# Performance work log

Measured on AMD Instinct MI355X. Metric: run time of the kernel, lower is better.

## Reference

```python
import jax, jax.numpy as jnp
import numpy as np

B, T, L, D = 4, 32, 64, 768
NHEAD, DFF, NLAYERS, NSPK = 12, 2048, 2, 4
DH = D // NHEAD


def setup_inputs() -> dict:
    key = jax.random.key(0)
    ks = jax.random.split(key, 12)
    s = 0.02
    return {
        "token_embeddings": jax.random.normal(ks[0], (B, T, L, D), jnp.float32) * s,
        "speaker_ids": jax.random.randint(ks[1], (B, T), 0, NSPK, jnp.int32),
        "Wq": jax.random.normal(ks[2], (D, D), jnp.float32) * s,
        "Wk": jax.random.normal(ks[3], (D, D), jnp.float32) * s,
        "Wv": jax.random.normal(ks[4], (D, D), jnp.float32) * s,
        "in_proj_w": jax.random.normal(ks[5], (NLAYERS, 3 * D, D), jnp.float32) * s,
        "in_proj_b": jnp.zeros((NLAYERS, 3 * D), jnp.float32),
        "out_w": jax.random.normal(ks[6], (NLAYERS, D, D), jnp.float32) * s,
        "out_b": jnp.zeros((NLAYERS, D), jnp.float32),
        "ln1_g": jnp.ones((NLAYERS, D), jnp.float32),
        "ln1_b": jnp.zeros((NLAYERS, D), jnp.float32),
        "ff1_w": jax.random.normal(ks[7], (NLAYERS, DFF, D), jnp.float32) * s,
        "ff1_b": jnp.zeros((NLAYERS, DFF), jnp.float32),
        "ff2_w": jax.random.normal(ks[8], (NLAYERS, D, DFF), jnp.float32) * s,
        "ff2_b": jnp.zeros((NLAYERS, D), jnp.float32),
        "ln2_g": jnp.ones((NLAYERS, D), jnp.float32),
        "ln2_b": jnp.zeros((NLAYERS, D), jnp.float32),
    }


def _layer_norm(x, g, b, eps=1e-5):
    mu = x.mean(-1, keepdims=True)
    var = ((x - mu) ** 2).mean(-1, keepdims=True)
    return (x - mu) * jax.lax.rsqrt(var + eps) * g + b


def _mha(x, w_in, b_in, w_out, b_out):
    # x: (N, L, D); torch nn.MultiheadAttention with in_proj/out_proj
    N, Lx, _ = x.shape
    qkv = x @ w_in.T + b_in  # (N, L, 3D)
    q, k, v = jnp.split(qkv, 3, axis=-1)
    def heads(z):
        return z.reshape(N, Lx, NHEAD, DH).transpose(0, 2, 1, 3)  # (N,H,L,dh)
    q, k, v = heads(q), heads(k), heads(v)
    scores = jnp.einsum("nhqd,nhkd->nhqk", q, k) / jnp.sqrt(jnp.float32(DH))
    attn = jax.nn.softmax(scores, axis=-1)
    out = jnp.einsum("nhqk,nhkd->nhqd", attn, v)
    out = out.transpose(0, 2, 1, 3).reshape(N, Lx, D)
    return out @ w_out.T + b_out


def reference(token_embeddings, speaker_ids, Wq, Wk, Wv, in_proj_w, in_proj_b,
              out_w, out_b, ln1_g, ln1_b, ff1_w, ff1_b, ff2_w, ff2_b, ln2_g, ln2_b):
    # edu embeddings: mean over token dim (frozen-BERT output stand-in)
    edu = token_embeddings.mean(axis=2)              # (B,T,D)
    tok = token_embeddings @ Wq.T                    # query_proj on tokens (B,T,L,D)
    k = edu @ Wk.T                                   # (B,T,D)
    v = edu @ Wv.T                                   # (B,T,D)
    # SAUTE: per-speaker causal cumulative sum of outer products k_u v_u^T
    same_spk = speaker_ids[:, :, None] == speaker_ids[:, None, :]
    causal = jnp.arange(T)[None, :, None] >= jnp.arange(T)[None, None, :]
    maskf = (same_spk & causal).astype(k.dtype)      # (B,T,T)
    M = jnp.einsum("btu,bui,buj->btij", maskf, k, v)  # (B,T,D,D) speaker state
    ctx = tok + jnp.einsum("btij,btlj->btli", M, tok)  # (B,T,L,D)
    # stacked post-norm TransformerEncoder (torch defaults: ReLU, dff=2048)
    x = ctx.reshape(B * T, L, D)
    for l in range(NLAYERS):
        a = _mha(x, in_proj_w[l], in_proj_b[l], out_w[l], out_b[l])
        x = _layer_norm(x + a, ln1_g[l], ln1_b[l])
        f = jax.nn.relu(x @ ff1_w[l].T + ff1_b[l]) @ ff2_w[l].T + ff2_b[l]
        x = _layer_norm(x + f, ln2_g[l], ln2_b[l])
    return x.reshape(B, T, L, D)
```

## Files before the change

kernel.cpp:

```cpp
#include <hip/hip_runtime.h>
#include <hip/hip_bf16.h>

#define BB 4
#define TT 32
#define LL 64
#define DD 768
#define NHEAD 12
#define DH 64
#define DFF 2048
#define NLAYERS 2
#define ROWS (BB*TT*LL)
#define BTN  (BB*TT)

typedef __attribute__((ext_vector_type(8))) short bf16x8;
typedef __attribute__((ext_vector_type(4))) float f32x4;

__device__ __forceinline__ int swz(int r, int c) {
    return r * 32 + ((c ^ ((r >> 1) & 3)) << 3);
}

__device__ __forceinline__ unsigned pack_bf16(float a, float b) {
    __hip_bfloat16 h0 = __float2bfloat16(a);
    __hip_bfloat16 h1 = __float2bfloat16(b);
    return (unsigned)*reinterpret_cast<unsigned short*>(&h0) |
           ((unsigned)*reinterpret_cast<unsigned short*>(&h1) << 16);
}

__device__ __forceinline__ short bf16s(float a) {
    __hip_bfloat16 h = __float2bfloat16(a);
    return *reinterpret_cast<short*>(&h);
}

struct CastArgs {
    const float* src[7];
    __hip_bfloat16* dst[7];
    int end[7];
};
__global__ __launch_bounds__(256) void cast_multi_kernel(CastArgs a)
{
    int q = blockIdx.x * 256 + threadIdx.x;
    if (q >= a.end[6]) return;
    int s = 0;
    while (q >= a.end[s]) ++s;
    int local = q - (s ? a.end[s - 1] : 0);
    float4 v = reinterpret_cast<const float4*>(a.src[s])[local];
    ushort4 o;
    __hip_bfloat16 h0 = __float2bfloat16(v.x);
    __hip_bfloat16 h1 = __float2bfloat16(v.y);
    __hip_bfloat16 h2 = __float2bfloat16(v.z);
    __hip_bfloat16 h3 = __float2bfloat16(v.w);
    o.x = *reinterpret_cast<unsigned short*>(&h0);
    o.y = *reinterpret_cast<unsigned short*>(&h1);
    o.z = *reinterpret_cast<unsigned short*>(&h2);
    o.w = *reinterpret_cast<unsigned short*>(&h3);
    reinterpret_cast<ushort4*>(a.dst[s])[local] = o;
}

__global__ __launch_bounds__(256) void te_prep_kernel(
    const float* __restrict__ te, __hip_bfloat16* __restrict__ teb,
    __hip_bfloat16* __restrict__ edu_b)
{
    int idx = blockIdx.x * 256 + threadIdx.x;
    int bt = idx / DD;
    int d  = idx - bt * DD;
    const float* p = te + ((size_t)bt * LL) * DD + d;
    __hip_bfloat16* q = teb + ((size_t)bt * LL) * DD + d;
    float s = 0.f;
#pragma unroll
    for (int l = 0; l < LL; ++l) {
        float v = p[(size_t)l * DD];
        s += v;
        q[(size_t)l * DD] = __float2bfloat16(v);
    }
    edu_b[idx] = __float2bfloat16(s * (1.0f / (float)LL));
}

template<int OUT_BF16, int RELU, int QKV>
__global__ __launch_bounds__(256) void gemm_bf16_kernel(
    const __hip_bfloat16* __restrict__ A,
    const __hip_bfloat16* __restrict__ B,
    const float* __restrict__ bias,
    void* __restrict__ Cout,
    __hip_bfloat16* __restrict__ Vout,
    int M, int N, int K, int ldC)
{
    __shared__ short lA[2][4096];
    __shared__ short lB[2][4096];
    const int tid  = threadIdx.x;
    const int lane = tid & 63;
    const int w    = tid >> 6;
    const int wr   = w >> 1, wc = w & 1;
    const int bm = blockIdx.y * 128;
    const int bn = blockIdx.x * 128;

    const int sr  = tid >> 2;
    const int cw  = tid & 3;
    const int sco = cw << 3;

    const int wo0 = swz(sr, cw);
    const int wo1 = swz(sr + 64, cw);
    int roA[4], roB[4];
#pragma unroll
    for (int m = 0; m < 4; ++m)
        roA[m] = swz(wr * 64 + m * 16 + (lane & 15), lane >> 4);
#pragma unroll
    for (int n = 0; n < 4; ++n)
        roB[n] = swz(wc * 64 + n * 16 + (lane & 15), lane >> 4);

    const short* Ag = reinterpret_cast<const short*>(A);
    const short* Bg = reinterpret_cast<const short*>(B);

    f32x4 acc[4][4] = {};

    bf16x8 ra0 = *reinterpret_cast<const bf16x8*>(Ag + (size_t)(bm + sr) * K + sco);
    bf16x8 ra1 = *reinterpret_cast<const bf16x8*>(Ag + (size_t)(bm + 64 + sr) * K + sco);
    bf16x8 rb0 = *reinterpret_cast<const bf16x8*>(Bg + (size_t)(bn + sr) * K + sco);
    bf16x8 rb1 = *reinterpret_cast<const bf16x8*>(Bg + (size_t)(bn + 64 + sr) * K + sco);
    *reinterpret_cast<bf16x8*>(&lA[0][wo0]) = ra0;
    *reinterpret_cast<bf16x8*>(&lA[0][wo1]) = ra1;
    *reinterpret_cast<bf16x8*>(&lB[0][wo0]) = rb0;
    *reinterpret_cast<bf16x8*>(&lB[0][wo1]) = rb1;
    __syncthreads();

    const int NT = K >> 5;
    int cur = 0;
    for (int t = 0; t < NT; ++t) {
        const bool nx = (t + 1 < NT);
        if (nx) {
            const int kn = (t + 1) << 5;
            ra0 = *reinterpret_cast<const bf16x8*>(Ag + (size_t)(bm + sr) * K + kn + sco);
            ra1 = *reinterpret_cast<const bf16x8*>(Ag + (size_t)(bm + 64 + sr) * K + kn + sco);
            rb0 = *reinterpret_cast<const bf16x8*>(Bg + (size_t)(bn + sr) * K + kn + sco);
            rb1 = *reinterpret_cast<const bf16x8*>(Bg + (size_t)(bn + 64 + sr) * K + kn + sco);
        }

        bf16x8 af[4], bfr[4];
#pragma unroll
        for (int m = 0; m < 4; ++m)
            af[m] = *reinterpret_cast<const bf16x8*>(&lA[cur][roA[m]]);
#pragma unroll
        for (int n = 0; n < 4; ++n)
            bfr[n] = *reinterpret_cast<const bf16x8*>(&lB[cur][roB[n]]);
#pragma unroll
        for (int m = 0; m < 4; ++m)
#pragma unroll
            for (int n = 0; n < 4; ++n)
                acc[m][n] = __builtin_amdgcn_mfma_f32_16x16x32_bf16(
                    af[m], bfr[n], acc[m][n], 0, 0, 0);

        if (nx) {
            *reinterpret_cast<bf16x8*>(&lA[cur ^ 1][wo0]) = ra0;
            *reinterpret_cast<bf16x8*>(&lA[cur ^ 1][wo1]) = ra1;
            *reinterpret_cast<bf16x8*>(&lB[cur ^ 1][wo0]) = rb0;
            *reinterpret_cast<bf16x8*>(&lB[cur ^ 1][wo1]) = rb1;
        }
        __syncthreads();
        cur ^= 1;
    }

    const int crow = (lane >> 4) * 4;
    const int ccol = lane & 15;
#pragma unroll
    for (int n = 0; n < 4; ++n) {
        const int col = bn + wc * 64 + n * 16 + ccol;
        const float bv = bias ? bias[col] : 0.f;
        if (QKV && col >= 1536) {
            const int hh = (col - 1536) >> 6;
            const int d  = (col - 1536) & 63;
#pragma unroll
            for (int m = 0; m < 4; ++m) {
                const int row0 = bm + wr * 64 + m * 16 + crow;
#pragma unroll
                for (int j = 0; j < 4; ++j) {
                    const int row = row0 + j;
                    const int ni = row >> 6, ll = row & 63;
                    Vout[(((size_t)ni * NHEAD + hh) << 12) + (d << 6) + ll] =
                        __float2bfloat16(acc[m][n][j] + bv);
                }
            }
        } else {
#pragma unroll
            for (int m = 0; m < 4; ++m) {
                const int row0 = bm + wr * 64 + m * 16 + crow;
#pragma unroll
                for (int j = 0; j < 4; ++j) {
                    float v = acc[m][n][j] + bv;
                    if (RELU) v = fmaxf(v, 0.f);
                    if (OUT_BF16)
                        reinterpret_cast<__hip_bfloat16*>(Cout)[(size_t)(row0 + j) * ldC + col] =
                            __float2bfloat16(v);
                    else
                        reinterpret_cast<float*>(Cout)[(size_t)(row0 + j) * ldC + col] = v;
                }
            }
        }
    }
}

__global__ __launch_bounds__(64) void attn_mfma_kernel(
    const __hip_bfloat16* __restrict__ qk,
    const __hip_bfloat16* __restrict__ vt,
    __hip_bfloat16* __restrict__ out)
{
    const int n = blockIdx.x, h = blockIdx.y;
    const int lane = threadIdx.x;
    const int lo = lane & 15, hi = lane >> 4;
    __shared__ short pl[64 * 72];

    const short* qg = reinterpret_cast<const short*>(qk) + (size_t)(n * 64) * 1536 + h * 64;

    f32x4 acc[4][4] = {};
#pragma unroll
    for (int ks = 0; ks < 2; ++ks) {
        const int kc = ks * 32 + hi * 8;
        bf16x8 af[4], bk[4];
#pragma unroll
        for (int m = 0; m < 4; ++m)
            af[m] = *reinterpret_cast<const bf16x8*>(qg + (size_t)(m * 16 + lo) * 1536 + kc);
#pragma unroll
        for (int nn = 0; nn < 4; ++nn)
            bk[nn] = *reinterpret_cast<const bf16x8*>(qg + 768 + (size_t)(nn * 16 + lo) * 1536 + kc);
#pragma unroll
        for (int m = 0; m < 4; ++m)
#pragma unroll
            for (int nn = 0; nn < 4; ++nn)
                acc[m][nn] = __builtin_amdgcn_mfma_f32_16x16x32_bf16(
                    af[m], bk[nn], acc[m][nn], 0, 0, 0);
    }

#pragma unroll
    for (int m = 0; m < 4; ++m) {
#pragma unroll
        for (int j = 0; j < 4; ++j) {
            float s0 = acc[m][0][j] * 0.125f;
            float s1 = acc[m][1][j] * 0.125f;
            float s2 = acc[m][2][j] * 0.125f;
            float s3 = acc[m][3][j] * 0.125f;
            float mx = fmaxf(fmaxf(s0, s1), fmaxf(s2, s3));
            mx = fmaxf(mx, __shfl_xor(mx, 1));
            mx = fmaxf(mx, __shfl_xor(mx, 2));
            mx = fmaxf(mx, __shfl_xor(mx, 4));
            mx = fmaxf(mx, __shfl_xor(mx, 8));
            float e0 = __expf(s0 - mx), e1 = __expf(s1 - mx);
            float e2 = __expf(s2 - mx), e3 = __expf(s3 - mx);
            float sm = e0 + e1 + e2 + e3;
            sm += __shfl_xor(sm, 1);
            sm += __shfl_xor(sm, 2);
            sm += __shfl_xor(sm, 4);
            sm += __shfl_xor(sm, 8);
            const float inv = 1.0f / sm;
            short* pr = &pl[(m * 16 + hi * 4 + j) * 72 + lo];
            pr[0]  = bf16s(e0 * inv);
            pr[16] = bf16s(e1 * inv);
            pr[32] = bf16s(e2 * inv);
            pr[48] = bf16s(e3 * inv);
        }
    }
    __syncthreads();

    const short* vg = reinterpret_cast<const short*>(vt) + ((size_t)(n * NHEAD + h) << 12);
    f32x4 o[4][4] = {};
#pragma unroll
    for (int ks = 0; ks < 2; ++ks) {
        const int kc = ks * 32 + hi * 8;
        bf16x8 pa[4], bv[4];
#pragma unroll
        for (int m = 0; m < 4; ++m)
            pa[m] = *reinterpret_cast<const bf16x8*>(&pl[(m * 16 + lo) * 72 + kc]);
#pragma unroll
        for (int nn = 0; nn < 4; ++nn)
            bv[nn] = *reinterpret_cast<const bf16x8*>(vg + (nn * 16 + lo) * 64 + kc);
#pragma unroll
        for (int m = 0; m < 4; ++m)
#pragma unroll
            for (int nn = 0; nn < 4; ++nn)
                o[m][nn] = __builtin_amdgcn_mfma_f32_16x16x32_bf16(
                    pa[m], bv[nn], o[m][nn], 0, 0, 0);
    }

#pragma unroll
    for (int m = 0; m < 4; ++m)
#pragma unroll
        for (int nn = 0; nn < 4; ++nn)
#pragma unroll
            for (int j = 0; j < 4; ++j)
                out[(size_t)(n * 64 + m * 16 + hi * 4 + j) * DD + h * 64 + nn * 16 + lo] =
                    __float2bfloat16(o[m][nn][j]);
}

__global__ __launch_bounds__(64) void saute_p_mfma_kernel(
    const __hip_bfloat16* __restrict__ Xb,
    const __hip_bfloat16* __restrict__ KV,
    const int* __restrict__ spk,
    __hip_bfloat16* __restrict__ P)
{
    const int lane = threadIdx.x;
    const int lo = lane & 15, hi = lane >> 4;
    const int row0 = blockIdx.x * 64;
    const int bt = row0 >> 6;
    const int b  = bt >> 5, t = bt & 31;

    const short* Ag = reinterpret_cast<const short*>(Xb) + (size_t)row0 * DD;
    const short* Bg = reinterpret_cast<const short*>(KV) + (size_t)(b * TT) * 1536 + 768;

    f32x4 acc[4][2] = {};
    for (int ks = 0; ks < 24; ++ks) {
        const int kc = ks * 32 + hi * 8;
        bf16x8 af[4], bv[2];
#pragma unroll
        for (int m = 0; m < 4; ++m)
            af[m] = *reinterpret_cast<const bf16x8*>(Ag + (size_t)(m * 16 + lo) * DD + kc);
#pragma unroll
        for (int nn = 0; nn < 2; ++nn)
            bv[nn] = *reinterpret_cast<const bf16x8*>(Bg + (size_t)(nn * 16 + lo) * 1536 + kc);
#pragma unroll
        for (int m = 0; m < 4; ++m)
#pragma unroll
            for (int nn = 0; nn < 2; ++nn)
                acc[m][nn] = __builtin_amdgcn_mfma_f32_16x16x32_bf16(
                    af[m], bv[nn], acc[m][nn], 0, 0, 0);
    }

    const int st = spk[bt];
#pragma unroll
    for (int nn = 0; nn < 2; ++nn) {
        const int u = nn * 16 + lo;
        const bool mk = (u <= t) && (spk[b * TT + u] == st);
#pragma unroll
        for (int m = 0; m < 4; ++m)
#pragma unroll
            for (int j = 0; j < 4; ++j) {
                const int row = row0 + m * 16 + hi * 4 + j;
                P[(size_t)row * 32 + u] =
                    mk ? __float2bfloat16(acc[m][nn][j]) : __float2bfloat16(0.f);
            }
    }
}

__global__ __launch_bounds__(256) void saute_ctx_kernel(
    __hip_bfloat16* __restrict__ Xb,
    const __hip_bfloat16* __restrict__ KV,
    const __hip_bfloat16* __restrict__ P)
{
    __shared__ unsigned kls[32 * 384];
    __shared__ float pls[8 * 32];
    const int row0 = blockIdx.x * 8;
    const int b = row0 >> 11;
    const int tid = threadIdx.x;

    const unsigned* k2 = reinterpret_cast<const unsigned*>(KV) + (size_t)(b * TT) * 768;
    for (int i = tid; i < 32 * 384; i += 256) {
        int u = i / 384, j = i - u * 384;
        kls[i] = k2[u * 768 + j];
    }
    pls[tid] = __bfloat162float(P[(size_t)row0 * 32 + tid]);
    __syncthreads();

    const int r = tid >> 5;
    const int l32 = tid & 31;
    unsigned* xrow = reinterpret_cast<unsigned*>(Xb + (size_t)(row0 + r) * DD);

    float2 acc[12];
#pragma unroll
    for (int c = 0; c < 12; ++c) {
        unsigned pk = xrow[l32 + 32 * c];
        acc[c].x = __uint_as_float(pk << 16);
        acc[c].y = __uint_as_float(pk & 0xffff0000u);
    }
    for (int u = 0; u < 32; ++u) {
        const float pv = pls[r * 32 + u];
        const unsigned* kr = &kls[u * 384];
#pragma unroll
        for (int c = 0; c < 12; ++c) {
            unsigned pk = kr[l32 + 32 * c];
            acc[c].x = fmaf(pv, __uint_as_float(pk << 16),          acc[c].x);
            acc[c].y = fmaf(pv, __uint_as_float(pk & 0xffff0000u), acc[c].y);
        }
    }
#pragma unroll
    for (int c = 0; c < 12; ++c)
        xrow[l32 + 32 * c] = pack_bf16(acc[c].x, acc[c].y);
}

template<int FINAL>
__global__ __launch_bounds__(192) void add_ln_kernel(
    __hip_bfloat16* __restrict__ xb, const __hip_bfloat16* __restrict__ y,
    const float* __restrict__ g, const float* __restrict__ bb,
    float* __restrict__ xf)
{
    const int row = blockIdx.x;
    const int tid = threadIdx.x;
    __shared__ float red[3];
    __shared__ float stat[2];
    const size_t base = (size_t)row * DD + tid * 4;

    uint2 xv = *reinterpret_cast<const uint2*>(xb + base);
    uint2 yv = *reinterpret_cast<const uint2*>(y + base);
    float v[4];
    v[0] = __uint_as_float(xv.x << 16)         + __uint_as_float(yv.x << 16);
    v[1] = __uint_as_float(xv.x & 0xffff0000u) + __uint_as_float(yv.x & 0xffff0000u);
    v[2] = __uint_as_float(xv.y << 16)         + __uint_as_float(yv.y << 16);
    v[3] = __uint_as_float(xv.y & 0xffff0000u) + __uint_as_float(yv.y & 0xffff0000u);

    float s = v[0] + v[1] + v[2] + v[3];
#pragma unroll
    for (int off = 32; off > 0; off >>= 1) s += __shfl_down(s, off);
    if ((tid & 63) == 0) red[tid >> 6] = s;
    __syncthreads();
    if (tid == 0) stat[0] = (red[0] + red[1] + red[2]) * (1.0f / (float)DD);
    __syncthreads();
    const float mu = stat[0];

    float d[4];
    float q = 0.f;
#pragma unroll
    for (int i = 0; i < 4; ++i) { d[i] = v[i] - mu; q += d[i] * d[i]; }
    __syncthreads();
#pragma unroll
    for (int off = 32; off > 0; off >>= 1) q += __shfl_down(q, off);
    if ((tid & 63) == 0) red[tid >> 6] = q;
    __syncthreads();
    if (tid == 0) stat[1] = (red[0] + red[1] + red[2]) * (1.0f / (float)DD);
    __syncthreads();
    const float rstd = rsqrtf(stat[1] + 1e-5f);

    float o[4];
#pragma unroll
    for (int i = 0; i < 4; ++i)
        o[i] = d[i] * rstd * g[tid * 4 + i] + bb[tid * 4 + i];

    if (FINAL) {
        float4 f4 = make_float4(o[0], o[1], o[2], o[3]);
        *reinterpret_cast<float4*>(xf + base) = f4;
    } else {
        uint2 ov;
        ov.x = pack_bf16(o[0], o[1]);
        ov.y = pack_bf16(o[2], o[3]);
        *reinterpret_cast<uint2*>(xb + base) = ov;
    }
}

extern "C" void kernel_launch(void* const* d_in, const int* in_sizes, int n_in,
                              void* d_out, int out_size, void* d_ws, size_t ws_size,
                              hipStream_t stream) {
    (void)in_sizes; (void)n_in; (void)out_size; (void)ws_size;
    const float* te  = (const float*)d_in[0];
    const int*   spk = (const int*)  d_in[1];
    const float* Wq  = (const float*)d_in[2];
    const float* Wk  = (const float*)d_in[3];
    const float* Wv  = (const float*)d_in[4];
    const float* ipw = (const float*)d_in[5];
    const float* ipb = (const float*)d_in[6];
    const float* ow  = (const float*)d_in[7];
    const float* ob  = (const float*)d_in[8];
    const float* g1  = (const float*)d_in[9];
    const float* b1  = (const float*)d_in[10];
    const float* f1w = (const float*)d_in[11];
    const float* f1b = (const float*)d_in[12];
    const float* f2w = (const float*)d_in[13];
    const float* f2b = (const float*)d_in[14];
    const float* g2  = (const float*)d_in[15];
    const float* b2  = (const float*)d_in[16];

    float* Xout = (float*)d_out;

    __hip_bfloat16* wsb   = (__hip_bfloat16*)d_ws;
    __hip_bfloat16* Wq_b  = wsb;
    __hip_bfloat16* ipw_b = Wq_b  + 589824;
    __hip_bfloat16* ow_b  = ipw_b + 3538944;
    __hip_bfloat16* f1w_b = ow_b  + 1179648;
    __hip_bfloat16* f2w_b = f1w_b + 3145728;
    __hip_bfloat16* Xb    = f2w_b + 3145728;
    __hip_bfloat16* SCR   = Xb    + 6291456;
    __hip_bfloat16* Vt    = SCR   + 12582912;
    __hip_bfloat16* Wkv_b = SCR;
    __hip_bfloat16* Ab    = SCR   + 18874368;
    __hip_bfloat16* Yb    = Ab    + 6291456;
    __hip_bfloat16* KV    = Yb    + 6291456;
    __hip_bfloat16* Pb    = KV    + 196608;
    __hip_bfloat16* edu_b = Pb    + 262144;

    te_prep_kernel<<<(BTN * DD) / 256, 256, 0, stream>>>(te, Ab, edu_b);

    CastArgs ca;
    ca.src[0] = Wq;  ca.dst[0] = Wq_b;
    ca.src[1] = ipw; ca.dst[1] = ipw_b;
    ca.src[2] = ow;  ca.dst[2] = ow_b;
    ca.src[3] = f1w; ca.dst[3] = f1w_b;
    ca.src[4] = f2w; ca.dst[4] = f2w_b;
    ca.src[5] = Wk;  ca.dst[5] = Wkv_b;
    ca.src[6] = Wv;  ca.dst[6] = Wkv_b + 589824;
    int quads[7] = {589824/4, 3538944/4, 1179648/4, 3145728/4, 3145728/4, 589824/4, 589824/4};
    int acc = 0;
    for (int i = 0; i < 7; ++i) { acc += quads[i]; ca.end[i] = acc; }
    cast_multi_kernel<<<(acc + 255) / 256, 256, 0, stream>>>(ca);

    gemm_bf16_kernel<1,0,0><<<dim3(1536/128, 1), 256, 0, stream>>>(
        edu_b, Wkv_b, nullptr, KV, nullptr, BTN, 1536, DD, 1536);

    gemm_bf16_kernel<1,0,0><<<dim3(DD/128, ROWS/128), 256, 0, stream>>>(
        Ab, Wq_b, nullptr, Xb, nullptr, ROWS, DD, DD, DD);

    saute_p_mfma_kernel<<<ROWS/64, 64, 0, stream>>>(Xb, KV, spk, Pb);
    saute_ctx_kernel<<<ROWS/8, 256, 0, stream>>>(Xb, KV, Pb);

    for (int l = 0; l < NLAYERS; ++l) {
        const __hip_bfloat16* ipw_l = ipw_b + (size_t)l * 3 * DD * DD;
        const __hip_bfloat16* ow_l  = ow_b  + (size_t)l * DD * DD;
        const __hip_bfloat16* f1w_l = f1w_b + (size_t)l * DFF * DD;
        const __hip_bfloat16* f2w_l = f2w_b + (size_t)l * DD * DFF;

        gemm_bf16_kernel<1,0,1><<<dim3(3*DD/128, ROWS/128), 256, 0, stream>>>(
            Xb, ipw_l, ipb + (size_t)l * 3 * DD, SCR, Vt, ROWS, 3*DD, DD, 1536);
        attn_mfma_kernel<<<dim3(BTN, NHEAD), 64, 0, stream>>>(SCR, Vt, Ab);
        gemm_bf16_kernel<1,0,0><<<dim3(DD/128, ROWS/128), 256, 0, stream>>>(
            Ab, ow_l, ob + (size_t)l * DD, Yb, nullptr, ROWS, DD, DD, DD);
        add_ln_kernel<0><<<ROWS, 192, 0, stream>>>(
            Xb, Yb, g1 + (size_t)l * DD, b1 + (size_t)l * DD, nullptr);
        gemm_bf16_kernel<1,1,0><<<dim3(DFF/128, ROWS/128), 256, 0, stream>>>(
            Xb, f1w_l, f1b + (size_t)l * DFF, SCR, nullptr, ROWS, DFF, DD, DFF);
        gemm_bf16_kernel<1,0,0><<<dim3(DD/128, ROWS/128), 256, 0, stream>>>(
            SCR, f2w_l, f2b + (size_t)l * DD, Yb, nullptr, ROWS, DD, DFF, DD);
        if (l == NLAYERS - 1)
            add_ln_kernel<1><<<ROWS, 192, 0, stream>>>(
                Xb, Yb, g2 + (size_t)l * DD, b2 + (size_t)l * DD, Xout);
        else
            add_ln_kernel<0><<<ROWS, 192, 0, stream>>>(
                Xb, Yb, g2 + (size_t)l * DD, b2 + (size_t)l * DD, nullptr);
    }
}
```

Measured before the change: 474.5 us.

## Add 256x128 GEMM tile for wide GEMMs and XCD-aware block swizzle

Adds a gemm_big_kernel with 256-row tiles (8x4 MFMA accumulators per wave) and uses it for the QKV and FF1 projections. This halves the number of blocks and raises operand reuse per loaded B tile. It also remaps block IDs across the 8 XCDs in all GEMMs so neighbouring tiles share an L2. The bigger tile roughly doubles register and LDS use, which may lower occupancy.

```diff
diff --git a/kernel.cpp b/kernel.cpp
--- a/kernel.cpp
+++ b/kernel.cpp
@@ -17,6 +17,12 @@
 
 __device__ __forceinline__ int swz(int r, int c) {
     return r * 32 + ((c ^ ((r >> 1) & 3)) << 3);
+}
+
+__device__ __forceinline__ int xcd_swizzle(int orig, int nwg) {
+    const int q8 = nwg >> 3, r8 = nwg & 7;
+    const int xcd = orig & 7, idx = orig >> 3;
+    return (xcd < r8 ? xcd * (q8 + 1) : r8 * (q8 + 1) + (xcd - r8) * q8) + idx;
 }
 
 __device__ __forceinline__ unsigned pack_bf16(float a, float b) {
@@ -90,8 +96,11 @@
     const int lane = tid & 63;
     const int w    = tid >> 6;
     const int wr   = w >> 1, wc = w & 1;
-    const int bm = blockIdx.y * 128;
-    const int bn = blockIdx.x * 128;
+
+    const int nbx = gridDim.x;
+    const int wg = xcd_swizzle(blockIdx.y * nbx + blockIdx.x, nbx * gridDim.y);
+    const int bm = (wg / nbx) * 128;
+    const int bn = (wg % nbx) * 128;
 
     const int sr  = tid >> 2;
     const int cw  = tid & 3;
@@ -182,6 +191,142 @@
 #pragma unroll
             for (int m = 0; m < 4; ++m) {
                 const int row0 = bm + wr * 64 + m * 16 + crow;
+#pragma unroll
+                for (int j = 0; j < 4; ++j) {
+                    float v = acc[m][n][j] + bv;
+                    if (RELU) v = fmaxf(v, 0.f);
+                    if (OUT_BF16)
+                        reinterpret_cast<__hip_bfloat16*>(Cout)[(size_t)(row0 + j) * ldC + col] =
+                            __float2bfloat16(v);
+                    else
+                        reinterpret_cast<float*>(Cout)[(size_t)(row0 + j) * ldC + col] = v;
+                }
+            }
+        }
+    }
+}
+
+template<int OUT_BF16, int RELU, int QKV>
+__global__ __launch_bounds__(256) void gemm_big_kernel(
+    const __hip_bfloat16* __restrict__ A,
+    const __hip_bfloat16* __restrict__ B,
+    const float* __restrict__ bias,
+    void* __restrict__ Cout,
+    __hip_bfloat16* __restrict__ Vout,
+    int M, int N, int K, int ldC)
+{
+    __shared__ short lA[2][8192];
+    __shared__ short lB[2][4096];
+    const int tid  = threadIdx.x;
+    const int lane = tid & 63;
+    const int w    = tid >> 6;
+    const int wr   = w >> 1, wc = w & 1;
+
+    const int nbx = gridDim.x;
+    const int wg = xcd_swizzle(blockIdx.y * nbx + blockIdx.x, nbx * gridDim.y);
+    const int bm = (wg / nbx) * 256;
+    const int bn = (wg % nbx) * 128;
+
+    const int sr  = tid >> 2;
+    const int cw  = tid & 3;
+    const int sco = cw << 3;
+
+    const int wa0 = swz(sr, cw);
+    const int wa1 = swz(sr + 64, cw);
+    const int wa2 = swz(sr + 128, cw);
+    const int wa3 = swz(sr + 192, cw);
+    const int wb0 = swz(sr, cw);
+    const int wb1 = swz(sr + 64, cw);
+    int roA[8], roB[4];
+#pragma unroll
+    for (int m = 0; m < 8; ++m)
+        roA[m] = swz(wr * 128 + m * 16 + (lane & 15), lane >> 4);
+#pragma unroll
+    for (int n = 0; n < 4; ++n)
+        roB[n] = swz(wc * 64 + n * 16 + (lane & 15), lane >> 4);
+
+    const short* Ag = reinterpret_cast<const short*>(A);
+    const short* Bg = reinterpret_cast<const short*>(B);
+
+    f32x4 acc[8][4] = {};
+
+    bf16x8 ra0 = *reinterpret_cast<const bf16x8*>(Ag + (size_t)(bm + sr) * K + sco);
+    bf16x8 ra1 = *reinterpret_cast<const bf16x8*>(Ag + (size_t)(bm + 64 + sr) * K + sco);
+    bf16x8 ra2 = *reinterpret_cast<const bf16x8*>(Ag + (size_t)(bm + 128 + sr) * K + sco);
+    bf16x8 ra3 = *reinterpret_cast<const bf16x8*>(Ag + (size_t)(bm + 192 + sr) * K + sco);
+    bf16x8 rb0 = *reinterpret_cast<const bf16x8*>(Bg + (size_t)(bn + sr) * K + sco);
+    bf16x8 rb1 = *reinterpret_cast<const bf16x8*>(Bg + (size_t)(bn + 64 + sr) * K + sco);
+    *reinterpret_cast<bf16x8*>(&lA[0][wa0]) = ra0;
+    *reinterpret_cast<bf16x8*>(&lA[0][wa1]) = ra1;
+    *reinterpret_cast<bf16x8*>(&lA[0][wa2]) = ra2;
+    *reinterpret_cast<bf16x8*>(&lA[0][wa3]) = ra3;
+    *reinterpret_cast<bf16x8*>(&lB[0][wb0]) = rb0;
+    *reinterpret_cast<bf16x8*>(&lB[0][wb1]) = rb1;
+    __syncthreads();
+
+    const int NT = K >> 5;
+    int cur = 0;
+    for (int t = 0; t < NT; ++t) {
+        const bool nx = (t + 1 < NT);
+        if (nx) {
+            const int kn = (t + 1) << 5;
+            ra0 = *reinterpret_cast<const bf16x8*>(Ag + (size_t)(bm + sr) * K + kn + sco);
+            ra1 = *reinterpret_cast<const bf16x8*>(Ag + (size_t)(bm + 64 + sr) * K + kn + sco);
+            ra2 = *reinterpret_cast<const bf16x8*>(Ag + (size_t)(bm + 128 + sr) * K + kn + sco);
+            ra3 = *reinterpret_cast<const bf16x8*>(Ag + (size_t)(bm + 192 + sr) * K + kn + sco);
+            rb0 = *reinterpret_cast<const bf16x8*>(Bg + (size_t)(bn + sr) * K + kn + sco);
+            rb1 = *reinterpret_cast<const bf16x8*>(Bg + (size_t)(bn + 64 + sr) * K + kn + sco);
+        }
+
+        bf16x8 bfr[4];
+#pragma unroll
+        for (int n = 0; n < 4; ++n)
+            bfr[n] = *reinterpret_cast<const bf16x8*>(&lB[cur][roB[n]]);
+#pragma unroll
+        for (int m = 0; m < 8; ++m) {
+            bf16x8 af = *reinterpret_cast<const bf16x8*>(&lA[cur][roA[m]]);
+#pragma unroll
+            for (int n = 0; n < 4; ++n)
+                acc[m][n] = __builtin_amdgcn_mfma_f32_16x16x32_bf16(
+                    af, bfr[n], acc[m][n], 0, 0, 0);
+        }
+
+        if (nx) {
+            *reinterpret_cast<bf16x8*>(&lA[cur ^ 1][wa0]) = ra0;
+            *reinterpret_cast<bf16x8*>(&lA[cur ^ 1][wa1]) = ra1;
+            *reinterpret_cast<bf16x8*>(&lA[cur ^ 1][wa2]) = ra2;
+            *reinterpret_cast<bf16x8*>(&lA[cur ^ 1][wa3]) = ra3;
+            *reinterpret_cast<bf16x8*>(&lB[cur ^ 1][wb0]) = rb0;
+            *reinterpret_cast<bf16x8*>(&lB[cur ^ 1][wb1]) = rb1;
+        }
+        __syncthreads();
+        cur ^= 1;
+    }
+
+    const int crow = (lane >> 4) * 4;
+    const int ccol = lane & 15;
+#pragma unroll
+    for (int n = 0; n < 4; ++n) {
+        const int col = bn + wc * 64 + n * 16 + ccol;
+        const float bv = bias ? bias[col] : 0.f;
+        if (QKV && col >= 1536) {
+            const int hh = (col - 1536) >> 6;
+            const int d  = (col - 1536) & 63;
+#pragma unroll
+            for (int m = 0; m < 8; ++m) {
+                const int row0 = bm + wr * 128 + m * 16 + crow;
+#pragma unroll
+                for (int j = 0; j < 4; ++j) {
+                    const int row = row0 + j;
+                    const int ni = row >> 6, ll = row & 63;
+                    Vout[(((size_t)ni * NHEAD + hh) << 12) + (d << 6) + ll] =
+                        __float2bfloat16(acc[m][n][j] + bv);
+                }
+            }
+        } else {
+#pragma unroll
+            for (int m = 0; m < 8; ++m) {
+                const int row0 = bm + wr * 128 + m * 16 + crow;
 #pragma unroll
                 for (int j = 0; j < 4; ++j) {
                     float v = acc[m][n][j] + bv;
@@ -510,14 +655,14 @@
         const __hip_bfloat16* f1w_l = f1w_b + (size_t)l * DFF * DD;
         const __hip_bfloat16* f2w_l = f2w_b + (size_t)l * DD * DFF;
 
-        gemm_bf16_kernel<1,0,1><<<dim3(3*DD/128, ROWS/128), 256, 0, stream>>>(
+        gemm_big_kernel<1,0,1><<<dim3(3*DD/128, ROWS/256), 256, 0, stream>>>(
             Xb, ipw_l, ipb + (size_t)l * 3 * DD, SCR, Vt, ROWS, 3*DD, DD, 1536);
         attn_mfma_kernel<<<dim3(BTN, NHEAD), 64, 0, stream>>>(SCR, Vt, Ab);
         gemm_bf16_kernel<1,0,0><<<dim3(DD/128, ROWS/128), 256, 0, stream>>>(
             Ab, ow_l, ob + (size_t)l * DD, Yb, nullptr, ROWS, DD, DD, DD);
         add_ln_kernel<0><<<ROWS, 192, 0, stream>>>(
             Xb, Yb, g1 + (size_t)l * DD, b1 + (size_t)l * DD, nullptr);
-        gemm_bf16_kernel<1,1,0><<<dim3(DFF/128, ROWS/128), 256, 0, stream>>>(
+        gemm_big_kernel<1,1,0><<<dim3(DFF/128, ROWS/256), 256, 0, stream>>>(
             Xb, f1w_l, f1b + (size_t)l * DFF, SCR, nullptr, ROWS, DFF, DD, DFF);
         gemm_bf16_kernel<1,0,0><<<dim3(DD/128, ROWS/128), 256, 0, stream>>>(
             SCR, f2w_l, f2b + (size_t)l * DD, Yb, nullptr, ROWS, DD, DFF, DD);
```

After: 490.9 us. +3.5%, slower.
